# Performance work log

Hardware: AMD Instinct MI355X
Metric: run time of the kernel (lower is better)

The kernel has to match this reference:

```python
import jax, jax.numpy as jnp
import numpy as np

N_NODES = 100000

def _inv_sqrt_deg(counts):
    # DGL norm='both': deg^{-1/2}, with 0-degree nodes mapped to 0
    return jnp.where(counts > 0, jax.lax.rsqrt(jnp.maximum(counts, 1.0)), 0.0)

def _graph_conv(x, src, dst, out_norm_src, in_norm_dst, W, b):
    # h = D_dst^{-1/2} A D_src^{-1/2} x W + b  (weight order commutes; apply after aggregation)
    xn = x * out_norm_src[:, None]                      # [N, d]
    msg = xn[src]                                       # gather [E, d]
    agg = jax.ops.segment_sum(msg, dst, num_segments=N_NODES)  # scatter-add [N, d]
    agg = agg * in_norm_dst[:, None]
    return agg @ W + b

def setup_inputs() -> dict:
    key = jax.random.key(0)
    ks = jax.random.split(key, 7)
    E = 1600000
    d_in, d_hid, d_out = 64, 64, 64
    x = jax.random.normal(ks[0], (N_NODES, d_in), dtype=jnp.float32)
    edge_src = jax.random.randint(ks[1], (E,), 0, N_NODES, dtype=jnp.int64)
    edge_dst = jax.random.randint(ks[2], (E,), 0, N_NODES, dtype=jnp.int64)
    W1 = jax.random.normal(ks[3], (d_in, d_hid), dtype=jnp.float32) * (1.0 / np.sqrt(d_in))
    b1 = jnp.zeros((d_hid,), dtype=jnp.float32)
    W2 = jax.random.normal(ks[4], (d_hid, d_out), dtype=jnp.float32) * (1.0 / np.sqrt(d_hid))
    b2 = jnp.zeros((d_out,), dtype=jnp.float32)
    return {"x": x, "edge_src": edge_src, "edge_dst": edge_dst,
            "W1": W1, "b1": b1, "W2": W2, "b2": b2}

def reference(x, edge_src, edge_dst, W1, b1, W2, b2):
    ones = jnp.ones(edge_src.shape, dtype=x.dtype)
    out_deg = jax.ops.segment_sum(ones, edge_src, num_segments=N_NODES)
    in_deg = jax.ops.segment_sum(ones, edge_dst, num_segments=N_NODES)
    src_norm = _inv_sqrt_deg(out_deg)
    dst_norm = _inv_sqrt_deg(in_deg)
    h = jax.nn.relu(_graph_conv(x, edge_src, edge_dst, src_norm, dst_norm, W1, b1))
    h = jax.nn.relu(_graph_conv(h, edge_src, edge_dst, src_norm, dst_norm, W2, b2))
    return h
```

## Files before the change

kernel.cpp:

```cpp
#include <hip/hip_runtime.h>
#include <hip/hip_bf16.h>

#define N_NODES 100000
#define DIM 64
#define SCAN_B 256

#define RANGE_NODES 50000
#define HWORDS 12500
#define HCHUNKS 64
#define SCHUNKS 256
#define BINSZ 512
#define NBINS 196

#define NBATCH 6250

typedef __attribute__((ext_vector_type(8))) short short8v;
typedef __attribute__((ext_vector_type(4))) float float4v;

__global__ __launch_bounds__(1024) void hist_kernel(
    const int* __restrict__ src, const int* __restrict__ dst, int nkeys,
    unsigned int* __restrict__ partials) {
  __shared__ unsigned int h[HWORDS];
  int which = blockIdx.x >> 7;
  int local = blockIdx.x & 127;
  int range = local >> 6;
  int chunk = local & 63;
  const int* keys = which ? dst : src;
  int lo = range * RANGE_NODES;
  for (int i = threadIdx.x; i < HWORDS; i += 1024) h[i] = 0;
  __syncthreads();
  int per = (((nkeys + HCHUNKS - 1) / HCHUNKS) + 3) & ~3;
  int beg = chunk * per;
  int end = min(beg + per, nkeys);
  int n4 = (end > beg) ? ((end - beg) >> 2) : 0;
  const int4* k4 = (const int4*)(keys + beg);
  for (int i = threadIdx.x; i < n4; i += 1024) {
    int4 kv = k4[i];
    int a = kv.x - lo, b = kv.y - lo, c = kv.z - lo, d = kv.w - lo;
    if ((unsigned)a < (unsigned)RANGE_NODES)
      atomicAdd(&h[a >> 2], 1u << ((a & 3) * 8));
    if ((unsigned)b < (unsigned)RANGE_NODES)
      atomicAdd(&h[b >> 2], 1u << ((b & 3) * 8));
    if ((unsigned)c < (unsigned)RANGE_NODES)
      atomicAdd(&h[c >> 2], 1u << ((c & 3) * 8));
    if ((unsigned)d < (unsigned)RANGE_NODES)
      atomicAdd(&h[d >> 2], 1u << ((d & 3) * 8));
  }
  for (int i = beg + (n4 << 2) + threadIdx.x; i < end; i += 1024) {
    int k = keys[i] - lo;
    if ((unsigned)k < (unsigned)RANGE_NODES)
      atomicAdd(&h[k >> 2], 1u << ((k & 3) * 8));
  }
  __syncthreads();
  unsigned int* outp = partials + (size_t)blockIdx.x * HWORDS;
  for (int i = threadIdx.x; i < HWORDS; i += 1024) outp[i] = h[i];
}

__global__ __launch_bounds__(256) void reduce_norm_kernel(
    const unsigned int* __restrict__ ps, const unsigned int* __restrict__ pd,
    float* __restrict__ sn, float* __restrict__ dn, int* __restrict__ ideg) {
  int w = blockIdx.x * 256 + threadIdx.x;
  if (w >= 2 * (N_NODES / 4)) return;
  int is_dst = (w >= N_NODES / 4);
  int lw = is_dst ? w - N_NODES / 4 : w;
  const unsigned int* p = is_dst ? pd : ps;
  int r = lw / HWORDS, wr = lw % HWORDS;
  const unsigned int* base = p + (size_t)(r * HCHUNKS) * HWORDS + wr;
  unsigned int s0 = 0, s1 = 0, s2 = 0, s3 = 0;
  for (int c = 0; c < HCHUNKS; ++c) {
    unsigned int v = base[(size_t)c * HWORDS];
    s0 += v & 255u; s1 += (v >> 8) & 255u; s2 += (v >> 16) & 255u; s3 += v >> 24;
  }
  unsigned int d[4] = {s0, s1, s2, s3};
  int n0 = r * RANGE_NODES + wr * 4;
#pragma unroll
  for (int j = 0; j < 4; ++j) {
    int n = n0 + j;
    float f = (d[j] > 0) ? rsqrtf((float)d[j]) : 0.0f;
    if (is_dst) { dn[n] = f; ideg[n] = (int)d[j]; }
    else        { sn[n] = f; }
  }
}

__global__ __launch_bounds__(256) void convert_prescale_kernel(
    const float* __restrict__ x, const float* __restrict__ sn,
    unsigned int* __restrict__ xb2, int nquads) {
  int i = blockIdx.x * 256 + threadIdx.x;
  if (i >= nquads) return;
  float s = sn[i >> 4];
  float4 v = ((const float4*)x)[i];
  __hip_bfloat162 a = __float22bfloat162_rn(make_float2(v.x * s, v.y * s));
  __hip_bfloat162 b = __float22bfloat162_rn(make_float2(v.z * s, v.w * s));
  unsigned int wa, wb;
  __builtin_memcpy(&wa, &a, 4);
  __builtin_memcpy(&wb, &b, 4);
  ((uint2*)xb2)[i] = make_uint2(wa, wb);
}

__global__ __launch_bounds__(SCAN_B) void scan_block_kernel(
    const int* __restrict__ in, int* __restrict__ out,
    int* __restrict__ bsum, int n) {
  __shared__ int s[SCAN_B];
  int t = threadIdx.x;
  int i = blockIdx.x * SCAN_B + t;
  int v = (i < n) ? in[i] : 0;
  s[t] = v;
  __syncthreads();
  for (int off = 1; off < SCAN_B; off <<= 1) {
    int add = (t >= off) ? s[t - off] : 0;
    __syncthreads();
    s[t] += add;
    __syncthreads();
  }
  if (i < n) out[i] = s[t] - v;
  if (t == SCAN_B - 1) bsum[blockIdx.x] = s[t];
}

__global__ __launch_bounds__(512) void scan_top_kernel(
    int* __restrict__ bsum, int nb) {
  __shared__ int s[512];
  int t = threadIdx.x;
  int v = (t < nb) ? bsum[t] : 0;
  s[t] = v;
  __syncthreads();
  for (int off = 1; off < 512; off <<= 1) {
    int add = (t >= off) ? s[t - off] : 0;
    __syncthreads();
    s[t] += add;
    __syncthreads();
  }
  if (t < nb) bsum[t] = s[t] - v;
}

__global__ __launch_bounds__(256) void scan_add_kernel(
    int* __restrict__ out, const int* __restrict__ bsum, int n, int total) {
  int i = blockIdx.x * blockDim.x + threadIdx.x;
  if (i < n) out[i] += bsum[i / SCAN_B];
  if (i == 0) out[n] = total;
}

__global__ __launch_bounds__(512) void bin_scatter_kernel(
    const int* __restrict__ src, const int* __restrict__ dst,
    const int* __restrict__ offsets, int* __restrict__ bin_cursor,
    int2* __restrict__ binned, int E) {
  __shared__ int cnt[NBINS];
  __shared__ int base[NBINS];
  int t = threadIdx.x;
  for (int i = t; i < NBINS; i += 512) cnt[i] = 0;
  __syncthreads();
  int per = (((E + SCHUNKS - 1) / SCHUNKS) + 3) & ~3;
  int beg = blockIdx.x * per;
  int end = min(beg + per, E);
  int n4 = (end > beg) ? ((end - beg) >> 2) : 0;
  const int4* d4 = (const int4*)(dst + beg);
  const int4* s4 = (const int4*)(src + beg);
  for (int i = t; i < n4; i += 512) {
    int4 dv = d4[i];
    atomicAdd(&cnt[dv.x >> 9], 1);
    atomicAdd(&cnt[dv.y >> 9], 1);
    atomicAdd(&cnt[dv.z >> 9], 1);
    atomicAdd(&cnt[dv.w >> 9], 1);
  }
  for (int i = beg + (n4 << 2) + t; i < end; i += 512)
    atomicAdd(&cnt[dst[i] >> 9], 1);
  __syncthreads();
  for (int i = t; i < NBINS; i += 512) {
    base[i] = offsets[i << 9] + atomicAdd(&bin_cursor[i], cnt[i]);
    cnt[i] = 0;
  }
  __syncthreads();
  for (int i = t; i < n4; i += 512) {
    int4 sv = s4[i];
    int4 dv = d4[i];
    int b0 = dv.x >> 9, r0 = atomicAdd(&cnt[b0], 1);
    binned[base[b0] + r0] = make_int2(sv.x, dv.x);
    int b1 = dv.y >> 9, r1 = atomicAdd(&cnt[b1], 1);
    binned[base[b1] + r1] = make_int2(sv.y, dv.y);
    int b2 = dv.z >> 9, r2 = atomicAdd(&cnt[b2], 1);
    binned[base[b2] + r2] = make_int2(sv.z, dv.z);
    int b3 = dv.w >> 9, r3 = atomicAdd(&cnt[b3], 1);
    binned[base[b3] + r3] = make_int2(sv.w, dv.w);
  }
  for (int i = beg + (n4 << 2) + t; i < end; i += 512) {
    int s = src[i], d = dst[i];
    int b = d >> 9;
    int r = atomicAdd(&cnt[b], 1);
    binned[base[b] + r] = make_int2(s, d);
  }
}

__global__ __launch_bounds__(512) void fill_binned_kernel(
    const int2* __restrict__ binned, const int* __restrict__ offsets,
    int* __restrict__ csr_src) {
  __shared__ int cur[BINSZ];
  __shared__ int offs[BINSZ];
  int b = blockIdx.x;
  int t = threadIdx.x;
  int lo = b << 9;
  for (int i = t; i < BINSZ; i += 512) {
    cur[i] = 0;
    offs[i] = offsets[min(lo + i, N_NODES)];
  }
  __syncthreads();
  int w0 = offsets[lo];
  int w1 = offsets[min(lo + BINSZ, N_NODES)];
  for (int e = w0 + t; e < w1; e += 512) {
    int2 sd = binned[e];
    int r = atomicAdd(&cur[sd.y - lo], 1);
    csr_src[offs[sd.y - lo] + r] = sd.x;
  }
}

__device__ __forceinline__ float bf_lo(unsigned int u) {
  unsigned int x = u << 16; float f; __builtin_memcpy(&f, &x, 4); return f;
}
__device__ __forceinline__ float bf_hi(unsigned int u) {
  unsigned int x = u & 0xffff0000u; float f; __builtin_memcpy(&f, &x, 4); return f;
}
__device__ __forceinline__ unsigned short bf16bits(float f) {
  __hip_bfloat16 h = __float2bfloat16(f);
  unsigned short u; __builtin_memcpy(&u, &h, 2); return u;
}
__device__ __forceinline__ void cvt_pair_hl(float x, float y,
                                            unsigned int& hi, unsigned int& lo) {
  unsigned int u0, u1;
  __builtin_memcpy(&u0, &x, 4);
  __builtin_memcpy(&u1, &y, 4);
  unsigned int h0 = u0 & 0xffff0000u, h1 = u1 & 0xffff0000u;
  hi = (h0 >> 16) | h1;
  float hf0, hf1;
  __builtin_memcpy(&hf0, &h0, 4);
  __builtin_memcpy(&hf1, &h1, 4);
  __hip_bfloat162 l2 = __float22bfloat162_rn(make_float2(x - hf0, y - hf1));
  __builtin_memcpy(&lo, &l2, 4);
}

__global__ __launch_bounds__(256) void stage_wfrag_kernel(
    const float* __restrict__ W1, const float* __restrict__ W2,
    short* __restrict__ Wg) {
  const float* W = blockIdx.x ? W2 : W1;
  short* outp = Wg + blockIdx.x * 8192;
  int t = threadIdx.x;
  for (int e = t; e < 1024; e += 256) {
    int lidx = e & 63;
    int f = e >> 6;
    int ktv = f & 1, ntv = (f >> 1) & 3, hl = f >> 3;
#pragma unroll
    for (int j = 0; j < 8; ++j) {
      int k = ktv * 32 + (lidx >> 4) * 8 + j;
      int c = ntv * 16 + (lidx & 15);
      float w = W[k * DIM + c];
      unsigned short hb = bf16bits(w);
      short val;
      if (hl == 0) {
        val = (short)hb;
      } else {
        unsigned int hx = (unsigned int)hb << 16;
        float hf; __builtin_memcpy(&hf, &hx, 4);
        val = (short)bf16bits(w - hf);
      }
      outp[e * 8 + j] = val;
    }
  }
}

template <bool PRESCALE, typename OUT_T>
__device__ __forceinline__ void epilogue_nt(
    float4v acc, float bv, int nb16, int kq, int lane, float snb,
    OUT_T* __restrict__ out, int nt) {
  int col = nt * 16 + (lane & 15);
#pragma unroll
  for (int r = 0; r < 4; ++r) {
    int node = nb16 + kq * 4 + r;
    float o = fmaxf(acc[r] + bv, 0.0f);
    if (PRESCALE) {
      o = o * __shfl(snb, kq * 4 + r);
      out[(long)node * DIM + col] = (OUT_T)__float2bfloat16(o);
    } else {
      out[(long)node * DIM + col] = (OUT_T)o;
    }
  }
}

template <bool PRESCALE, typename OUT_T>
__global__ __launch_bounds__(256, 4) void fused_layer_kernel(
    const __hip_bfloat16* __restrict__ xb, const int* __restrict__ csr_src,
    const int* __restrict__ offsets, const float* __restrict__ sn,
    const float* __restrict__ dn, const short* __restrict__ Wg,
    const float* __restrict__ bias, OUT_T* __restrict__ out, int N) {
  __shared__ __align__(16) float Astage[4][16][64];

  int t = threadIdx.x;
  int lane = t & 63;
  int wslot = t >> 6;
  int g = lane >> 4;
  int q = lane & 15;

  float bias_nt[4];
#pragma unroll
  for (int nt = 0; nt < 4; ++nt) bias_nt[nt] = bias[nt * 16 + q];

  const uint2* __restrict__ xr = (const uint2*)xb;
  const short8v* __restrict__ wfrag = (const short8v*)Wg;
  char* abase = (char*)&Astage[wslot][0][0];

  int nwaves = gridDim.x * 4;
  for (int nb = blockIdx.x * 4 + wslot; nb < NBATCH; nb += nwaves) {
    asm volatile("" ::: "memory");
    int nb16 = nb * 16;
    int offv = offsets[nb16 + min(lane, 16)];
    float dnv = dn[nb16 + q];
    float snb = PRESCALE ? sn[nb16 + q] : 0.0f;

    for (int ni = 0; ni < 16; ++ni) {
      int beg = __shfl(offv, ni);
      int end = __shfl(offv, ni + 1);
      float a0 = 0.f, a1 = 0.f, a2 = 0.f, a3 = 0.f;
      for (int base = beg; base < end; base += 16) {
        int j0 = base + g;
        int jm = end - 1;
        bool p0 = j0 < end, p1 = j0 + 4 < end, p2 = j0 + 8 < end,
             p3 = j0 + 12 < end;
        int s0 = csr_src[min(j0, jm)];
        int s1 = csr_src[min(j0 + 4, jm)];
        int s2 = csr_src[min(j0 + 8, jm)];
        int s3 = csr_src[min(j0 + 12, jm)];
        uint2 v0 = make_uint2(0u, 0u), v1 = v0, v2 = v0, v3 = v0;
        if (p0) v0 = xr[(size_t)s0 * 16 + q];
        if (p1) v1 = xr[(size_t)s1 * 16 + q];
        if (p2) v2 = xr[(size_t)s2 * 16 + q];
        if (p3) v3 = xr[(size_t)s3 * 16 + q];
        a0 += bf_lo(v0.x); a1 += bf_hi(v0.x); a2 += bf_lo(v0.y); a3 += bf_hi(v0.y);
        a0 += bf_lo(v1.x); a1 += bf_hi(v1.x); a2 += bf_lo(v1.y); a3 += bf_hi(v1.y);
        a0 += bf_lo(v2.x); a1 += bf_hi(v2.x); a2 += bf_lo(v2.y); a3 += bf_hi(v2.y);
        a0 += bf_lo(v3.x); a1 += bf_hi(v3.x); a2 += bf_lo(v3.y); a3 += bf_hi(v3.y);
      }
      a0 += __shfl_xor(a0, 16); a1 += __shfl_xor(a1, 16);
      a2 += __shfl_xor(a2, 16); a3 += __shfl_xor(a3, 16);
      a0 += __shfl_xor(a0, 32); a1 += __shfl_xor(a1, 32);
      a2 += __shfl_xor(a2, 32); a3 += __shfl_xor(a3, 32);

      float dnw = __shfl(dnv, ni);
      if (lane < 16) {
        int woff = ni * 256 + ((lane * 16) ^ ((ni & 15) << 4));
        *(float4*)(abase + woff) =
            make_float4(a0 * dnw, a1 * dnw, a2 * dnw, a3 * dnw);
      }
    }

    float4v acc0 = {0.f, 0.f, 0.f, 0.f}, acc1 = acc0, acc2 = acc0, acc3 = acc0;
#pragma unroll
    for (int kt = 0; kt < 2; ++kt) {
      int o1 = kt * 128 + g * 32;
      float4 fa = *(const float4*)(abase + q * 256 + (o1 ^ (q << 4)));
      float4 fb = *(const float4*)(abase + q * 256 + ((o1 + 16) ^ (q << 4)));
      union { unsigned int w[4]; short8v v; } Uh, Ul;
      cvt_pair_hl(fa.x, fa.y, Uh.w[0], Ul.w[0]);
      cvt_pair_hl(fa.z, fa.w, Uh.w[1], Ul.w[1]);
      cvt_pair_hl(fb.x, fb.y, Uh.w[2], Ul.w[2]);
      cvt_pair_hl(fb.z, fb.w, Uh.w[3], Ul.w[3]);
      short8v ahi = Uh.v, alo = Ul.v;
#define PROJ_NT(NT, ACC)                                                      \
      {                                                                       \
        short8v bh = wfrag[(((NT) * 2) + kt) * 64 + lane];                    \
        short8v bl = wfrag[(((4 + (NT)) * 2) + kt) * 64 + lane];              \
        ACC = __builtin_amdgcn_mfma_f32_16x16x32_bf16(ahi, bh, ACC, 0, 0, 0); \
        ACC = __builtin_amdgcn_mfma_f32_16x16x32_bf16(alo, bh, ACC, 0, 0, 0); \
        ACC = __builtin_amdgcn_mfma_f32_16x16x32_bf16(ahi, bl, ACC, 0, 0, 0); \
      }
      PROJ_NT(0, acc0)
      PROJ_NT(1, acc1)
      PROJ_NT(2, acc2)
      PROJ_NT(3, acc3)
#undef PROJ_NT
    }

    float snbv = PRESCALE ? snb : 0.0f;
    epilogue_nt<PRESCALE, OUT_T>(acc0, bias_nt[0], nb16, g, lane, snbv, out, 0);
    epilogue_nt<PRESCALE, OUT_T>(acc1, bias_nt[1], nb16, g, lane, snbv, out, 1);
    epilogue_nt<PRESCALE, OUT_T>(acc2, bias_nt[2], nb16, g, lane, snbv, out, 2);
    epilogue_nt<PRESCALE, OUT_T>(acc3, bias_nt[3], nb16, g, lane, snbv, out, 3);
  }
}

extern "C" void kernel_launch(void* const* d_in, const int* in_sizes, int n_in,
                              void* d_out, int out_size, void* d_ws, size_t ws_size,
                              hipStream_t stream) {
  const float* x        = (const float*)d_in[0];
  const int*   edge_src = (const int*)d_in[1];
  const int*   edge_dst = (const int*)d_in[2];
  const float* W1       = (const float*)d_in[3];
  const float* b1       = (const float*)d_in[4];
  const float* W2       = (const float*)d_in[5];
  const float* b2       = (const float*)d_in[6];
  float* out = (float*)d_out;

  const int E = in_sizes[1];
  const int N = N_NODES;
  const int NB = (N + SCAN_B - 1) / SCAN_B;

  float* sn         = (float*)d_ws;
  float* dn         = sn + N;
  int*   ideg       = (int*)(dn + N);
  int*   offsets    = ideg + N;
  int*   bsum       = offsets + (N + 1);
  int*   bin_cursor = bsum + 512;
  int*   csr_src    = bin_cursor + 256;
  unsigned int* xb_raw = (unsigned int*)(csr_src + E);
  unsigned int* regionB = xb_raw + (size_t)N * DIM / 2;
  unsigned int* partials = regionB;
  int2*  binned   = (int2*)regionB;
  __hip_bfloat16* xb  = (__hip_bfloat16*)xb_raw;
  __hip_bfloat16* h1b = (__hip_bfloat16*)regionB;
  short* Wg = (short*)ideg;

  hipMemsetAsync(bin_cursor, 0, 256 * sizeof(int), stream);

  hist_kernel<<<256, 1024, 0, stream>>>(edge_src, edge_dst, E, partials);
  reduce_norm_kernel<<<(2 * (N / 4) + 255) / 256, 256, 0, stream>>>(
      partials, partials + (size_t)128 * HWORDS, sn, dn, ideg);

  {
    int nquads = N * DIM / 4;
    convert_prescale_kernel<<<(nquads + 255) / 256, 256, 0, stream>>>(
        x, sn, xb_raw, nquads);
  }

  scan_block_kernel<<<NB, SCAN_B, 0, stream>>>(ideg, offsets, bsum, N);
  stage_wfrag_kernel<<<2, 256, 0, stream>>>(W1, W2, Wg);
  scan_top_kernel<<<1, 512, 0, stream>>>(bsum, NB);
  scan_add_kernel<<<(N + 255) / 256, 256, 0, stream>>>(offsets, bsum, N, E);

  bin_scatter_kernel<<<SCHUNKS, 512, 0, stream>>>(edge_src, edge_dst, offsets,
                                                  bin_cursor, binned, E);
  fill_binned_kernel<<<NBINS, 512, 0, stream>>>(binned, offsets, csr_src);

  const int fb = 1024;

  fused_layer_kernel<true, __hip_bfloat16><<<fb, 256, 0, stream>>>(
      xb, csr_src, offsets, sn, dn, Wg, b1, h1b, N);

  fused_layer_kernel<false, float><<<fb, 256, 0, stream>>>(
      h1b, csr_src, offsets, sn, dn, Wg + 8192, b2, out, N);
}
```

Measured before the change: 222.3 us.

## Replace shared-memory histogram with global atomic degree counting and fuse scan stages

Replaces the two-pass histogram (per-chunk packed byte counters in LDS plus a reduction kernel) with one kernel that does global atomicAdd on int degree arrays. The rsqrt normalisation moves into the block scan kernel, and the top-level scan is merged into the scan-add kernel, so each block redundantly rescans the block sums in LDS. Together these cut several launches and the traffic of writing and reading the partial histograms. In exchange, 3.2M global atomics over 100K addresses may contend, and two memsets are added.

```diff
diff --git a/kernel.cpp b/kernel.cpp
--- a/kernel.cpp
+++ b/kernel.cpp
@@ -5,9 +5,6 @@
 #define DIM 64
 #define SCAN_B 256
 
-#define RANGE_NODES 50000
-#define HWORDS 12500
-#define HCHUNKS 64
 #define SCHUNKS 256
 #define BINSZ 512
 #define NBINS 196
@@ -17,68 +14,25 @@
 typedef __attribute__((ext_vector_type(8))) short short8v;
 typedef __attribute__((ext_vector_type(4))) float float4v;
 
-__global__ __launch_bounds__(1024) void hist_kernel(
-    const int* __restrict__ src, const int* __restrict__ dst, int nkeys,
-    unsigned int* __restrict__ partials) {
-  __shared__ unsigned int h[HWORDS];
-  int which = blockIdx.x >> 7;
-  int local = blockIdx.x & 127;
-  int range = local >> 6;
-  int chunk = local & 63;
-  const int* keys = which ? dst : src;
-  int lo = range * RANGE_NODES;
-  for (int i = threadIdx.x; i < HWORDS; i += 1024) h[i] = 0;
-  __syncthreads();
-  int per = (((nkeys + HCHUNKS - 1) / HCHUNKS) + 3) & ~3;
-  int beg = chunk * per;
-  int end = min(beg + per, nkeys);
-  int n4 = (end > beg) ? ((end - beg) >> 2) : 0;
-  const int4* k4 = (const int4*)(keys + beg);
-  for (int i = threadIdx.x; i < n4; i += 1024) {
-    int4 kv = k4[i];
-    int a = kv.x - lo, b = kv.y - lo, c = kv.z - lo, d = kv.w - lo;
-    if ((unsigned)a < (unsigned)RANGE_NODES)
-      atomicAdd(&h[a >> 2], 1u << ((a & 3) * 8));
-    if ((unsigned)b < (unsigned)RANGE_NODES)
-      atomicAdd(&h[b >> 2], 1u << ((b & 3) * 8));
-    if ((unsigned)c < (unsigned)RANGE_NODES)
-      atomicAdd(&h[c >> 2], 1u << ((c & 3) * 8));
-    if ((unsigned)d < (unsigned)RANGE_NODES)
-      atomicAdd(&h[d >> 2], 1u << ((d & 3) * 8));
-  }
-  for (int i = beg + (n4 << 2) + threadIdx.x; i < end; i += 1024) {
-    int k = keys[i] - lo;
-    if ((unsigned)k < (unsigned)RANGE_NODES)
-      atomicAdd(&h[k >> 2], 1u << ((k & 3) * 8));
-  }
-  __syncthreads();
-  unsigned int* outp = partials + (size_t)blockIdx.x * HWORDS;
-  for (int i = threadIdx.x; i < HWORDS; i += 1024) outp[i] = h[i];
-}
-
-__global__ __launch_bounds__(256) void reduce_norm_kernel(
-    const unsigned int* __restrict__ ps, const unsigned int* __restrict__ pd,
-    float* __restrict__ sn, float* __restrict__ dn, int* __restrict__ ideg) {
-  int w = blockIdx.x * 256 + threadIdx.x;
-  if (w >= 2 * (N_NODES / 4)) return;
-  int is_dst = (w >= N_NODES / 4);
-  int lw = is_dst ? w - N_NODES / 4 : w;
-  const unsigned int* p = is_dst ? pd : ps;
-  int r = lw / HWORDS, wr = lw % HWORDS;
-  const unsigned int* base = p + (size_t)(r * HCHUNKS) * HWORDS + wr;
-  unsigned int s0 = 0, s1 = 0, s2 = 0, s3 = 0;
-  for (int c = 0; c < HCHUNKS; ++c) {
-    unsigned int v = base[(size_t)c * HWORDS];
-    s0 += v & 255u; s1 += (v >> 8) & 255u; s2 += (v >> 16) & 255u; s3 += v >> 24;
-  }
-  unsigned int d[4] = {s0, s1, s2, s3};
-  int n0 = r * RANGE_NODES + wr * 4;
-#pragma unroll
-  for (int j = 0; j < 4; ++j) {
-    int n = n0 + j;
-    float f = (d[j] > 0) ? rsqrtf((float)d[j]) : 0.0f;
-    if (is_dst) { dn[n] = f; ideg[n] = (int)d[j]; }
-    else        { sn[n] = f; }
+__global__ __launch_bounds__(256) void degree_kernel(
+    const int* __restrict__ src, const int* __restrict__ dst, int E,
+    int* __restrict__ odeg, int* __restrict__ ideg) {
+  int stride = gridDim.x * 256;
+  int E4 = E >> 2;
+  const int4* s4 = (const int4*)src;
+  const int4* d4 = (const int4*)dst;
+  for (int i = blockIdx.x * 256 + threadIdx.x; i < E4; i += stride) {
+    int4 sv = s4[i];
+    int4 dv = d4[i];
+    atomicAdd(&odeg[sv.x], 1); atomicAdd(&odeg[sv.y], 1);
+    atomicAdd(&odeg[sv.z], 1); atomicAdd(&odeg[sv.w], 1);
+    atomicAdd(&ideg[dv.x], 1); atomicAdd(&ideg[dv.y], 1);
+    atomicAdd(&ideg[dv.z], 1); atomicAdd(&ideg[dv.w], 1);
+  }
+  for (int i = (E4 << 2) + blockIdx.x * 256 + threadIdx.x; i < E;
+       i += stride) {
+    atomicAdd(&odeg[src[i]], 1);
+    atomicAdd(&ideg[dst[i]], 1);
   }
 }
 
@@ -98,12 +52,18 @@
 }
 
 __global__ __launch_bounds__(SCAN_B) void scan_block_kernel(
-    const int* __restrict__ in, int* __restrict__ out,
-    int* __restrict__ bsum, int n) {
+    const int* __restrict__ ideg, const int* __restrict__ odeg,
+    float* __restrict__ sn, float* __restrict__ dn,
+    int* __restrict__ out, int* __restrict__ bsum, int n) {
   __shared__ int s[SCAN_B];
   int t = threadIdx.x;
   int i = blockIdx.x * SCAN_B + t;
-  int v = (i < n) ? in[i] : 0;
+  int v = (i < n) ? ideg[i] : 0;
+  if (i < n) {
+    dn[i] = (v > 0) ? rsqrtf((float)v) : 0.0f;
+    int o = odeg[i];
+    sn[i] = (o > 0) ? rsqrtf((float)o) : 0.0f;
+  }
   s[t] = v;
   __syncthreads();
   for (int off = 1; off < SCAN_B; off <<= 1) {
@@ -116,9 +76,11 @@
   if (t == SCAN_B - 1) bsum[blockIdx.x] = s[t];
 }
 
-__global__ __launch_bounds__(512) void scan_top_kernel(
-    int* __restrict__ bsum, int nb) {
+__global__ __launch_bounds__(512) void scan_add_kernel(
+    int* __restrict__ out, const int* __restrict__ bsum, int nb, int n,
+    int total) {
   __shared__ int s[512];
+  __shared__ int ex[512];
   int t = threadIdx.x;
   int v = (t < nb) ? bsum[t] : 0;
   s[t] = v;
@@ -129,13 +91,10 @@
     s[t] += add;
     __syncthreads();
   }
-  if (t < nb) bsum[t] = s[t] - v;
-}
-
-__global__ __launch_bounds__(256) void scan_add_kernel(
-    int* __restrict__ out, const int* __restrict__ bsum, int n, int total) {
-  int i = blockIdx.x * blockDim.x + threadIdx.x;
-  if (i < n) out[i] += bsum[i / SCAN_B];
+  ex[t] = s[t] - v;
+  __syncthreads();
+  int i = blockIdx.x * 512 + t;
+  if (i < n) out[i] += ex[i >> 8];
   if (i == 0) out[n] = total;
 }
 
@@ -402,23 +361,26 @@
   float* sn         = (float*)d_ws;
   float* dn         = sn + N;
   int*   ideg       = (int*)(dn + N);
-  int*   offsets    = ideg + N;
+  int*   bin_cursor = ideg + N;
+  int*   offsets    = bin_cursor + 256;
   int*   bsum       = offsets + (N + 1);
-  int*   bin_cursor = bsum + 512;
-  int*   csr_src    = bin_cursor + 256;
+  int*   csr_src    = bsum + 512;
   unsigned int* xb_raw = (unsigned int*)(csr_src + E);
   unsigned int* regionB = xb_raw + (size_t)N * DIM / 2;
-  unsigned int* partials = regionB;
+  int*   odeg     = (int*)regionB;
   int2*  binned   = (int2*)regionB;
   __hip_bfloat16* xb  = (__hip_bfloat16*)xb_raw;
   __hip_bfloat16* h1b = (__hip_bfloat16*)regionB;
   short* Wg = (short*)ideg;
 
-  hipMemsetAsync(bin_cursor, 0, 256 * sizeof(int), stream);
-
-  hist_kernel<<<256, 1024, 0, stream>>>(edge_src, edge_dst, E, partials);
-  reduce_norm_kernel<<<(2 * (N / 4) + 255) / 256, 256, 0, stream>>>(
-      partials, partials + (size_t)128 * HWORDS, sn, dn, ideg);
+  hipMemsetAsync(ideg, 0, (N + 256) * sizeof(int), stream);
+  hipMemsetAsync(odeg, 0, N * sizeof(int), stream);
+
+  degree_kernel<<<1024, 256, 0, stream>>>(edge_src, edge_dst, E, odeg, ideg);
+
+  scan_block_kernel<<<NB, SCAN_B, 0, stream>>>(ideg, odeg, sn, dn,
+                                               offsets, bsum, N);
+  stage_wfrag_kernel<<<2, 256, 0, stream>>>(W1, W2, Wg);
 
   {
     int nquads = N * DIM / 4;
@@ -426,10 +388,7 @@
         x, sn, xb_raw, nquads);
   }
 
-  scan_block_kernel<<<NB, SCAN_B, 0, stream>>>(ideg, offsets, bsum, N);
-  stage_wfrag_kernel<<<2, 256, 0, stream>>>(W1, W2, Wg);
-  scan_top_kernel<<<1, 512, 0, stream>>>(bsum, NB);
-  scan_add_kernel<<<(N + 255) / 256, 256, 0, stream>>>(offsets, bsum, N, E);
+  scan_add_kernel<<<(N + 511) / 512, 512, 0, stream>>>(offsets, bsum, NB, N, E);
 
   bin_scatter_kernel<<<SCHUNKS, 512, 0, stream>>>(edge_src, edge_dst, offsets,
                                                   bin_cursor, binned, E);
```

After: 337.6 us. 1.52x slower.
